# Performance work log

Measured on AMD Instinct MI355X. Metric: run time of the kernel, lower is better.

The kernel has to match this reference:

```python
import jax, jax.numpy as jnp
import numpy as np

# PaTH attention (training path, attention_mask=None):
#   score(t,s) = q_t^T (H_t H_{t-1} ... H_{s+1}) k_s,  H_i = I - beta_i w_i w_i^T (w_i unit-norm)
# computed in closed form via a UT/WY-style triangular solve, then causal softmax with
# FoX-style forget gate: logits += cumsum(logsigmoid(g))_t - cumsum(logsigmoid(g))_s.

NUM_HEADS = 32
HEAD_DIM = 64
CONV_K = 3
NEG_INF = -1e30


def _forward(hidden_states, Wq, Wk, Wv, Ww1, Ww2, conv_w, Wbt, bbt, Wg, bg, Wo):
    B, T, D = hidden_states.shape
    H, hd, Kc = NUM_HEADS, HEAD_DIM, CONV_K
    h = hidden_states
    q = h @ Wq                                   # [B,T,D]
    k = h @ Wk
    v = h @ Wv
    w = (h @ Ww1) @ Ww2                          # low-rank w_proj (rank 32)
    beta = jax.nn.sigmoid(h @ Wbt + bbt) * 2.0   # [B,T,H], in (0,2)
    g = jax.nn.log_sigmoid(h @ Wg + bg)          # [B,T,H] forget gate (log-space)
    # causal depthwise short conv (kernel 3, no bias) + silu on w
    wp = jnp.pad(w, ((0, 0), (Kc - 1, 0), (0, 0)))
    w = sum(wp[:, j:j + T, :] * conv_w[:, j] for j in range(Kc))
    w = jax.nn.silu(w)
    split = lambda x: x.reshape(B, T, H, hd)
    q, k, v, w = split(q), split(k), split(v), split(w)
    w = w * jax.lax.rsqrt(jnp.sum(w * w, axis=-1, keepdims=True))  # l2_norm per head
    # pairwise inner products, [B,H,T,S]
    Dqk = jnp.einsum('bthd,bshd->bhts', q, k)
    E = jnp.einsum('bthd,bshd->bhts', q, w)
    S = jnp.einsum('bthd,bshd->bhts', w, k)
    L = jnp.einsum('bthd,bshd->bhts', w, w)
    bcol = jnp.transpose(beta, (0, 2, 1))[:, :, None, :]  # beta_i indexed by column i
    strict = jnp.tril(jnp.ones((T, T), bool), -1)
    # C[t,s] = w_t^T (H_{t-1}...H_{s+1}) k_s solves (I + strict(L) diag(beta)) C = strict(S)
    M = jnp.eye(T, dtype=q.dtype) + jnp.where(strict, L * bcol, 0.0)
    rhs = jnp.where(strict, S, 0.0)
    C = jax.scipy.linalg.solve_triangular(M, rhs, lower=True, unit_diagonal=True)
    causal = jnp.tril(jnp.ones((T, T), bool))
    # A[t,s] = q_t^T k_s - sum_{s<i<=t} (q_t^T w_i) beta_i C[i,s]
    EB = jnp.where(causal, E, 0.0) * bcol
    A = Dqk - EB @ C
    G = jnp.cumsum(jnp.transpose(g, (0, 2, 1)), axis=-1)  # [B,H,T]
    logits = A * (hd ** -0.5) + G[..., :, None] - G[..., None, :]
    logits = jnp.where(causal, logits, NEG_INF)
    P = jax.nn.softmax(logits, axis=-1)
    o = jnp.einsum('bhts,bshd->bthd', P, v).reshape(B, T, D)
    return o @ Wo


def setup_inputs() -> dict:
    key = jax.random.key(0)
    ks = jax.random.split(key, 12)
    B, T, D, H, Kc = 1, 1024, 2048, NUM_HEADS, CONV_K
    r = lambda k, shape, scale: jax.random.normal(k, shape, dtype=jnp.float32) * scale
    s = D ** -0.5
    return {
        'hidden_states': r(ks[0], (B, T, D), 1.0),
        'Wq': r(ks[1], (D, D), s),
        'Wk': r(ks[2], (D, D), s),
        'Wv': r(ks[3], (D, D), s),
        'Ww1': r(ks[4], (D, 32), s),
        'Ww2': r(ks[5], (32, D), 32 ** -0.5),
        'conv_w': r(ks[6], (D, Kc), Kc ** -0.5),
        'Wbt': r(ks[7], (D, H), s),
        'bbt': r(ks[8], (H,), 1.0),
        'Wg': r(ks[9], (D, H), s),
        'bg': r(ks[10], (H,), 1.0),
        'Wo': r(ks[11], (D, D), s),
    }


def reference(hidden_states, Wq, Wk, Wv, Ww1, Ww2, conv_w, Wbt, bbt, Wg, bg, Wo):
    return _forward(hidden_states, Wq, Wk, Wv, Ww1, Ww2, conv_w, Wbt, bbt, Wg, bg, Wo)
```

## Files before the change

### kernel.cpp

```cpp
#include <hip/hip_runtime.h>
#include <hip/hip_bf16.h>

typedef __hip_bfloat16 bf16;
typedef unsigned short ushort_t;

#define T_  1024
#define D_  2048
#define H_  32
#define HD_ 64

static const size_t TT_ = (size_t)T_ * T_;
static const size_t TD_ = (size_t)T_ * D_;

__device__ __forceinline__ ushort_t f2bf(float v) {
    bf16 b = __float2bfloat16(v);
    return *(ushort_t*)&b;
}
__device__ __forceinline__ float bf2f(ushort_t u) {
    bf16 b = *(bf16*)&u;
    return __bfloat162float(b);
}

typedef __attribute__((ext_vector_type(8))) short frag8;
typedef __attribute__((ext_vector_type(4))) float f32x4;
typedef __attribute__((ext_vector_type(4))) unsigned short u16x4;
typedef __attribute__((ext_vector_type(8))) unsigned short u16x8;

#define MFMA16(a, b, c) __builtin_amdgcn_mfma_f32_16x16x32_bf16((a), (b), (c), 0, 0, 0)

template <int OUT>
__global__ __launch_bounds__(256) void mfma_gemm(
    const ushort_t* __restrict__ A, const ushort_t* __restrict__ Bt,
    void* __restrict__ Cout, void* __restrict__ Cout2, int M, int N, int K)
{
    __shared__ short Al[128 * 32];
    __shared__ short Bl[128 * 32];
    int tid = threadIdx.x;
    int w = tid >> 6, l = tid & 63;
    int row0 = blockIdx.y * 128, col0 = blockIdx.x * 128;
    int mq = (w >> 1) * 64, nq = (w & 1) * 64;
    int lm = l & 15, kq = l >> 4;
    f32x4 acc[4][4] = {};
    const ushort_t* Ap = A + (size_t)row0 * K;
    const ushort_t* Bp = Bt + (size_t)col0 * K;
    for (int kk = 0; kk < K; kk += 32) {
        __syncthreads();
#pragma unroll
        for (int r = 0; r < 2; r++) {
            int c = r * 256 + w * 64 + l;
            int row = c >> 2, kc = (c & 3) * 8;
            const ushort_t* ga = Ap + (size_t)row * K + kk + kc;
            const ushort_t* gb = Bp + (size_t)row * K + kk + kc;
            short* la = Al + (size_t)(r * 256 + w * 64) * 8;
            short* lb = Bl + (size_t)(r * 256 + w * 64) * 8;
            __builtin_amdgcn_global_load_lds((const __attribute__((address_space(1))) void*)ga,
                                             (__attribute__((address_space(3))) void*)la, 16, 0, 0);
            __builtin_amdgcn_global_load_lds((const __attribute__((address_space(1))) void*)gb,
                                             (__attribute__((address_space(3))) void*)lb, 16, 0, 0);
        }
        __builtin_amdgcn_s_waitcnt(0);
        __syncthreads();
        frag8 af[4], bfg[4];
#pragma unroll
        for (int i = 0; i < 4; i++)
            af[i] = *(const frag8*)&Al[(size_t)(mq + i * 16 + lm) * 32 + kq * 8];
#pragma unroll
        for (int j = 0; j < 4; j++)
            bfg[j] = *(const frag8*)&Bl[(size_t)(nq + j * 16 + lm) * 32 + kq * 8];
#pragma unroll
        for (int i = 0; i < 4; i++)
#pragma unroll
            for (int j = 0; j < 4; j++)
                acc[i][j] = MFMA16(af[i], bfg[j], acc[i][j]);
    }
#pragma unroll
    for (int i = 0; i < 4; i++)
#pragma unroll
        for (int j = 0; j < 4; j++)
#pragma unroll
            for (int r = 0; r < 4; r++) {
                int row = row0 + mq + i * 16 + kq * 4 + r;
                int col = col0 + nq + j * 16 + lm;
                float v = acc[i][j][r];
                if (OUT == 0) {
                    ((float*)Cout)[(size_t)row * N + col] = v;
                } else {
                    ushort_t* q = (ushort_t*)Cout;
                    int which = col >> 11, cl = col & 2047;
                    int hd = cl >> 6, d = cl & 63;
                    if (which == 0)
                        q[((size_t)hd * M + row) * 64 + d] = f2bf(v);
                    else if (which == 1)
                        q[(size_t)M * 2048 + ((size_t)hd * M + row) * 64 + d] = f2bf(v);
                    else if (which == 2)
                        q[(size_t)M * 4096 + ((size_t)hd * 64 + d) * M + row] = f2bf(v);
                    else
                        ((float*)Cout2)[(size_t)row * 128 + (col - 6144)] = v;
                }
            }
}

__global__ void transpose_convert(const float* __restrict__ W, ushort_t* __restrict__ Wt,
                                  int R, int Cc)
{
    __shared__ float tile[32][33];
    int bx = blockIdx.x * 32, by = blockIdx.y * 32;
    int tx = threadIdx.x, ty = threadIdx.y;
    for (int i = ty; i < 32; i += 8)
        tile[i][tx] = W[(size_t)(by + i) * Cc + bx + tx];
    __syncthreads();
    for (int i = ty; i < 32; i += 8)
        Wt[(size_t)(bx + i) * R + by + tx] = f2bf(tile[tx][i]);
}

__global__ void pack96(const float* __restrict__ Ww1, const float* __restrict__ Wbt,
                       const float* __restrict__ Wg, ushort_t* __restrict__ dst)
{
    int r = blockIdx.x;
    int k = blockIdx.y * 256 + threadIdx.x;
    float v = 0.f;
    if (r < 32)       v = Ww1[(size_t)k * 32 + r];
    else if (r < 64)  v = Wbt[(size_t)k * 32 + (r - 32)];
    else if (r < 96)  v = Wg[(size_t)k * 32 + (r - 64)];
    dst[(size_t)r * 2048 + k] = f2bf(v);
}

__global__ void convert_bf16(const float* __restrict__ in, ushort_t* __restrict__ out, int n)
{
    int i = blockIdx.x * 256 + threadIdx.x;
    if (i < n) out[i] = f2bf(in[i]);
}

__global__ void bg96(const float* __restrict__ s96, const float* __restrict__ bbt,
                     const float* __restrict__ bgp, ushort_t* __restrict__ w1bf,
                     float* __restrict__ betaB, float* __restrict__ Gb)
{
    int idx = blockIdx.x * 256 + threadIdx.x;
    int t = idx >> 7, o = idx & 127;
    if (o >= 96) return;
    float v = s96[(size_t)t * 128 + o];
    if (o < 32) {
        w1bf[(size_t)t * 32 + o] = f2bf(v);
    } else if (o < 64) {
        float xb = v + bbt[o - 32];
        betaB[(size_t)t * H_ + (o - 32)] = 2.f / (1.f + expf(-xb));
    } else {
        float xg = v + bgp[o - 64];
        Gb[(size_t)t * H_ + (o - 64)] =
            (xg >= 0.f) ? -log1pf(expf(-xg)) : (xg - log1pf(expf(xg)));
    }
}

__global__ void scan_g(float* __restrict__ G)
{
    int h = blockIdx.x;
    int tid = threadIdx.x;
    __shared__ float psum[256];
    float v[4];
    float s = 0.f;
#pragma unroll
    for (int r = 0; r < 4; r++) {
        v[r] = G[(size_t)(tid * 4 + r) * H_ + h];
        s += v[r];
    }
    psum[tid] = s;
    __syncthreads();
    for (int off = 1; off < 256; off <<= 1) {
        float t = (tid >= off) ? psum[tid - off] : 0.f;
        __syncthreads();
        psum[tid] += t;
        __syncthreads();
    }
    float run = (tid > 0) ? psum[tid - 1] : 0.f;
#pragma unroll
    for (int r = 0; r < 4; r++) {
        run += v[r];
        G[(size_t)(tid * 4 + r) * H_ + h] = run;
    }
}

__global__ void conv_silu_norm(const float* __restrict__ wr, const float* __restrict__ convw,
                               ushort_t* __restrict__ wh)
{
    int b = blockIdx.x;
    int t = b >> 5, h = b & 31;
    int d = threadIdx.x;
    int c = h * 64 + d;
    float c0 = convw[c * 3 + 0];
    float c1 = convw[c * 3 + 1];
    float c2 = convw[c * 3 + 2];
    float x = c2 * wr[(size_t)t * D_ + c];
    if (t >= 1) x += c1 * wr[(size_t)(t - 1) * D_ + c];
    if (t >= 2) x += c0 * wr[(size_t)(t - 2) * D_ + c];
    float y = x / (1.f + expf(-x));
    float ss = y * y;
    for (int off = 32; off > 0; off >>= 1) ss += __shfl_xor(ss, off, 64);
    wh[((size_t)h * T_ + t) * 64 + d] = f2bf(y * rsqrtf(ss));
}

__global__ __launch_bounds__(256) void pairdotLC(
    const ushort_t* __restrict__ kh, const ushort_t* __restrict__ wh,
    const float* __restrict__ betaB,
    ushort_t* __restrict__ ELb, ushort_t* __restrict__ Ct, int hs)
{
    int s0 = blockIdx.x * 64, t0 = blockIdx.y * 64, z = blockIdx.z;
    if (s0 > t0) return;
    int head = hs + z;
    const ushort_t* kb = kh + (size_t)head * T_ * 64;
    const ushort_t* wb = wh + (size_t)head * T_ * 64;
    ushort_t* Lz = ELb + (size_t)z * TT_;
    ushort_t* Cz = Ct + (size_t)z * TT_;
    int tid = threadIdx.x;
    int w = tid >> 6, l = tid & 63;
    int lm = l & 15, kq = l >> 4;
    int rowA = t0 + w * 16 + lm;
    f32x4 accL[4] = {}, accS[4] = {};
#pragma unroll
    for (int kk = 0; kk < 64; kk += 32) {
        frag8 aw = *(const frag8*)&wb[(size_t)rowA * 64 + kk + kq * 8];
#pragma unroll
        for (int j = 0; j < 4; j++) {
            int colr = s0 + j * 16 + lm;
            frag8 bw = *(const frag8*)&wb[(size_t)colr * 64 + kk + kq * 8];
            frag8 bk = *(const frag8*)&kb[(size_t)colr * 64 + kk + kq * 8];
            accL[j] = MFMA16(aw, bw, accL[j]);
            accS[j] = MFMA16(aw, bk, accS[j]);
        }
    }
    int m0 = w * 16 + kq * 4;
#pragma unroll
    for (int j = 0; j < 4; j++) {
        int s = s0 + j * 16 + lm;
        float beta = betaB[(size_t)s * H_ + head];
        ushort_t cl[4];
#pragma unroll
        for (int r = 0; r < 4; r++) {
            int t = t0 + m0 + r;
            Lz[(size_t)t * T_ + s] = f2bf((s < t) ? accL[j][r] * beta : 0.f);
            cl[r] = f2bf((s < t) ? accS[j][r] : 0.f);
        }
        *(u16x4*)&Cz[(size_t)s * T_ + t0 + m0] = *(u16x4*)cl;
    }
}

__global__ __launch_bounds__(256) void pairdotE(
    const ushort_t* __restrict__ qh, const ushort_t* __restrict__ wh,
    const float* __restrict__ betaB, ushort_t* __restrict__ ELb, int hs)
{
    int s0 = blockIdx.x * 64, t0 = blockIdx.y * 64, z = blockIdx.z;
    if (s0 > t0) return;
    int head = hs + z;
    const ushort_t* qb = qh + (size_t)head * T_ * 64;
    const ushort_t* wb = wh + (size_t)head * T_ * 64;
    ushort_t* Ez = ELb + (size_t)z * TT_;
    int tid = threadIdx.x;
    int w = tid >> 6, l = tid & 63;
    int lm = l & 15, kq = l >> 4;
    int rowA = t0 + w * 16 + lm;
    f32x4 accE[4] = {};
#pragma unroll
    for (int kk = 0; kk < 64; kk += 32) {
        frag8 aq = *(const frag8*)&qb[(size_t)rowA * 64 + kk + kq * 8];
#pragma unroll
        for (int j = 0; j < 4; j++) {
            frag8 bw = *(const frag8*)&wb[(size_t)(s0 + j * 16 + lm) * 64 + kk + kq * 8];
            accE[j] = MFMA16(aq, bw, accE[j]);
        }
    }
    int m0 = w * 16 + kq * 4;
#pragma unroll
    for (int j = 0; j < 4; j++) {
        int s = s0 + j * 16 + lm;
        float beta = betaB[(size_t)s * H_ + head];
#pragma unroll
        for (int r = 0; r < 4; r++) {
            int t = t0 + m0 + r;
            Ez[(size_t)t * T_ + s] = f2bf((s <= t) ? -accE[j][r] * beta : 0.f);
        }
    }
}

__global__ void diag_inv(const ushort_t* __restrict__ Lb, ushort_t* __restrict__ Minv)
{
    int bi = blockIdx.x, z = blockIdx.y;
    const ushort_t* Lh = Lb + (size_t)z * TT_;
    __shared__ float Nb[64][65];
    __shared__ float Xc[64][65];
    int tid = threadIdx.x;
    for (int i = tid; i < 4096; i += 64) {
        int r = i >> 6, c = i & 63;
        Nb[r][c] = (c < r) ? bf2f(Lh[(size_t)(bi * 64 + r) * T_ + bi * 64 + c]) : 0.f;
    }
    __syncthreads();
    int j = tid;
    for (int t = 0; t < 64; t++) {
        float v = (t == j) ? 1.f : 0.f;
        for (int i = j; i < t; i++) v -= Nb[t][i] * Xc[i][j];
        Xc[t][j] = v;
    }
    __syncthreads();
    ushort_t* Mo = Minv + ((size_t)z * 16 + bi) * 4096;
    for (int i = tid; i < 4096; i += 64) Mo[i] = f2bf(Xc[i >> 6][i & 63]);
}

__global__ __launch_bounds__(256) void solve_mfma(
    ushort_t* __restrict__ Ct, const ushort_t* __restrict__ Lb,
    const ushort_t* __restrict__ Minv)
{
    int ct = blockIdx.x, z = blockIdx.y;
    ushort_t* Cz = Ct + (size_t)z * TT_;
    const ushort_t* Lz = Lb + (size_t)z * TT_;
    __shared__ ushort_t Cl[64][136];
    __shared__ ushort_t Ll[64][136];
    __shared__ ushort_t Xbt[64][72];
    int tid = threadIdx.x;
    int w = tid >> 6, l = tid & 63;
    int lm = l & 15, kq = l >> 4;
    int s0 = ct * 64;
    int m0 = w * 16 + kq * 4;
    for (int bi = ct; bi < 16; bi++) {
        f32x4 acc[4] = {};
        for (int kkc = s0; kkc < bi * 64; kkc += 128) {
            int len = bi * 64 - kkc; if (len > 128) len = 128;
            int lsh = (len == 128) ? 4 : 3;
            __syncthreads();
            for (int i = tid; i < (64 << lsh); i += 256) {
                int r = i >> lsh, c = (i & ((1 << lsh) - 1)) * 8;
                *(u16x8*)&Cl[r][c] = *(const u16x8*)&Cz[(size_t)(s0 + r) * T_ + kkc + c];
                *(u16x8*)&Ll[r][c] = *(const u16x8*)&Lz[(size_t)(bi * 64 + r) * T_ + kkc + c];
            }
            __syncthreads();
            for (int kk2 = 0; kk2 < len; kk2 += 32) {
                frag8 a = *(const frag8*)&Ll[w * 16 + lm][kk2 + kq * 8];
#pragma unroll
                for (int j = 0; j < 4; j++) {
                    frag8 b = *(const frag8*)&Cl[j * 16 + lm][kk2 + kq * 8];
                    acc[j] = MFMA16(a, b, acc[j]);
                }
            }
        }
        __syncthreads();
#pragma unroll
        for (int j = 0; j < 4; j++) {
            int sc = s0 + j * 16 + lm;
            u16x4 rhs = *(const u16x4*)&Cz[(size_t)sc * T_ + bi * 64 + m0];
            ushort_t xb[4];
#pragma unroll
            for (int r = 0; r < 4; r++) xb[r] = f2bf(bf2f(rhs[r]) - acc[j][r]);
            *(u16x4*)&Xbt[j * 16 + lm][m0] = *(u16x4*)xb;
        }
        __syncthreads();
        f32x4 res[4] = {};
        const ushort_t* Mo = Minv + ((size_t)z * 16 + bi) * 4096;
#pragma unroll
        for (int kk = 0; kk < 64; kk += 32) {
            frag8 a = *(const frag8*)&Mo[(size_t)(w * 16 + lm) * 64 + kk + kq * 8];
#pragma unroll
            for (int j = 0; j < 4; j++) {
                frag8 b = *(const frag8*)&Xbt[j * 16 + lm][kk + kq * 8];
                res[j] = MFMA16(a, b, res[j]);
            }
        }
#pragma unroll
        for (int j = 0; j < 4; j++) {
            int sc = s0 + j * 16 + lm;
            ushort_t cr[4];
#pragma unroll
            for (int r = 0; r < 4; r++) cr[r] = f2bf(res[j][r]);
            *(u16x4*)&Cz[(size_t)sc * T_ + bi * 64 + m0] = *(u16x4*)cr;
        }
        __syncthreads();
    }
}

__global__ __launch_bounds__(256) void flash_attn(
    const ushort_t* __restrict__ qh, const ushort_t* __restrict__ kh,
    const ushort_t* __restrict__ vt, const ushort_t* __restrict__ Em,
    const ushort_t* __restrict__ Ct, const float* __restrict__ Gb,
    ushort_t* __restrict__ of, int hs)
{
    int tb = (int)gridDim.x - 1 - (int)blockIdx.x;
    int z = blockIdx.y;
    int t0 = tb * 64;
    int head = hs + z;
    const ushort_t* qb = qh + (size_t)head * T_ * 64;
    const ushort_t* kb = kh + (size_t)head * T_ * 64;
    const ushort_t* vb = vt + (size_t)head * 64 * T_;
    const ushort_t* Ez = Em + (size_t)z * TT_;
    const ushort_t* Cz = Ct + (size_t)z * TT_;
    __shared__ ushort_t Kl[64][72];
    __shared__ ushort_t Vl[64][72];
    __shared__ ushort_t Cl[64][72];
    __shared__ ushort_t El[64][72];
    __shared__ ushort_t Pl[4][16][72];
    int tid = threadIdx.x;
    int w = tid >> 6, l = tid & 63;
    int lm = l & 15, kq = l >> 4;
    int rowA = t0 + w * 16 + lm;
    int m0 = w * 16 + kq * 4;
    frag8 aq0 = *(const frag8*)&qb[(size_t)rowA * 64 + kq * 8];
    frag8 aq1 = *(const frag8*)&qb[(size_t)rowA * 64 + 32 + kq * 8];
    f32x4 o[4] = {};
    float mrow[4], lrow[4];
#pragma unroll
    for (int r = 0; r < 4; r++) { mrow[r] = -1e30f; lrow[r] = 0.f; }
    for (int st = 0; st <= tb; st++) {
        int s0 = st * 64;
        __syncthreads();
        for (int i = tid; i < 512; i += 256) {
            int r = i >> 3, c = (i & 7) * 8;
            *(u16x8*)&Kl[r][c] = *(const u16x8*)&kb[(size_t)(s0 + r) * 64 + c];
            *(u16x8*)&Vl[r][c] = *(const u16x8*)&vb[(size_t)r * T_ + s0 + c];
        }
        __syncthreads();
        f32x4 x[4] = {};
#pragma unroll
        for (int j = 0; j < 4; j++) {
            frag8 b0 = *(const frag8*)&Kl[j * 16 + lm][kq * 8];
            frag8 b1 = *(const frag8*)&Kl[j * 16 + lm][32 + kq * 8];
            x[j] = MFMA16(aq0, b0, x[j]);
            x[j] = MFMA16(aq1, b1, x[j]);
        }
        for (int kkc = s0; kkc < t0 + 64; kkc += 64) {
            __syncthreads();
            for (int i = tid; i < 512; i += 256) {
                int r = i >> 3, c = (i & 7) * 8;
                *(u16x8*)&Cl[r][c] = *(const u16x8*)&Cz[(size_t)(s0 + r) * T_ + kkc + c];
                *(u16x8*)&El[r][c] = *(const u16x8*)&Ez[(size_t)(t0 + r) * T_ + kkc + c];
            }
            __syncthreads();
#pragma unroll
            for (int kk2 = 0; kk2 < 64; kk2 += 32) {
                frag8 a = *(const frag8*)&El[w * 16 + lm][kk2 + kq * 8];
#pragma unroll
                for (int j = 0; j < 4; j++) {
                    frag8 b = *(const frag8*)&Cl[j * 16 + lm][kk2 + kq * 8];
                    x[j] = MFMA16(a, b, x[j]);
                }
            }
        }
        float lg[4][4];
#pragma unroll
        for (int j = 0; j < 4; j++) {
            int s = s0 + j * 16 + lm;
            float g = Gb[(size_t)s * H_ + head];
#pragma unroll
            for (int r = 0; r < 4; r++) {
                int t = t0 + m0 + r;
                lg[j][r] = (s <= t) ? (x[j][r] * 0.125f - g) : -1e30f;
            }
        }
        float rmax[4];
#pragma unroll
        for (int r = 0; r < 4; r++)
            rmax[r] = fmaxf(fmaxf(lg[0][r], lg[1][r]), fmaxf(lg[2][r], lg[3][r]));
#pragma unroll
        for (int d = 1; d < 16; d <<= 1)
#pragma unroll
            for (int r = 0; r < 4; r++) rmax[r] = fmaxf(rmax[r], __shfl_xor(rmax[r], d, 64));
        float mnew[4], alpha[4];
#pragma unroll
        for (int r = 0; r < 4; r++) {
            mnew[r] = fmaxf(mrow[r], rmax[r]);
            alpha[r] = __expf(mrow[r] - mnew[r]);
            mrow[r] = mnew[r];
        }
        float rsum[4] = {0.f, 0.f, 0.f, 0.f};
#pragma unroll
        for (int j = 0; j < 4; j++)
#pragma unroll
            for (int r = 0; r < 4; r++) {
                float p = __expf(lg[j][r] - mnew[r]);
                lg[j][r] = p;
                rsum[r] += p;
            }
#pragma unroll
        for (int d = 1; d < 16; d <<= 1)
#pragma unroll
            for (int r = 0; r < 4; r++) rsum[r] += __shfl_xor(rsum[r], d, 64);
#pragma unroll
        for (int r = 0; r < 4; r++) lrow[r] = lrow[r] * alpha[r] + rsum[r];
#pragma unroll
        for (int j = 0; j < 4; j++)
#pragma unroll
            for (int r = 0; r < 4; r++) o[j][r] *= alpha[r];
#pragma unroll
        for (int j = 0; j < 4; j++)
#pragma unroll
            for (int r = 0; r < 4; r++)
                Pl[w][kq * 4 + r][j * 16 + lm] = f2bf(lg[j][r]);
#pragma unroll
        for (int j = 0; j < 4; j++) {
            frag8 b0 = *(const frag8*)&Vl[j * 16 + lm][kq * 8];
            frag8 b1 = *(const frag8*)&Vl[j * 16 + lm][32 + kq * 8];
            frag8 a0 = *(const frag8*)&Pl[w][lm][kq * 8];
            frag8 a1 = *(const frag8*)&Pl[w][lm][32 + kq * 8];
            o[j] = MFMA16(a0, b0, o[j]);
            o[j] = MFMA16(a1, b1, o[j]);
        }
    }
#pragma unroll
    for (int j = 0; j < 4; j++) {
        int col = head * 64 + j * 16 + lm;
#pragma unroll
        for (int r = 0; r < 4; r++) {
            int t = t0 + m0 + r;
            of[(size_t)t * D_ + col] = f2bf(o[j][r] / lrow[r]);
        }
    }
}

extern "C" void kernel_launch(void* const* d_in, const int* in_sizes, int n_in,
                              void* d_out, int out_size, void* d_ws, size_t ws_size,
                              hipStream_t stream)
{
    const float* h     = (const float*)d_in[0];
    const float* Wq    = (const float*)d_in[1];
    const float* Wk    = (const float*)d_in[2];
    const float* Wv    = (const float*)d_in[3];
    const float* Ww1   = (const float*)d_in[4];
    const float* Ww2   = (const float*)d_in[5];
    const float* convw = (const float*)d_in[6];
    const float* Wbt   = (const float*)d_in[7];
    const float* bbt   = (const float*)d_in[8];
    const float* Wg    = (const float*)d_in[9];
    const float* bgp   = (const float*)d_in[10];
    const float* Wo    = (const float*)d_in[11];
    float* out = (float*)d_out;

    float* ws = (float*)d_ws;
    size_t off = 0;
    auto allocF = [&](size_t nf) { float* p = ws + off; off += (nf + 1023) & ~(size_t)1023; return p; };

    float*    wr    = allocF(TD_);
    float*    s96   = allocF((size_t)T_ * 128);
    float*    betaB = allocF((size_t)T_ * H_);
    float*    Gb    = allocF((size_t)T_ * H_);
    ushort_t* h_bf  = (ushort_t*)allocF(TD_ / 2);
    ushort_t* of_bf = h_bf;
    ushort_t* w1bf  = (ushort_t*)allocF((size_t)T_ * 32 / 2);
    ushort_t* Ww2t  = (ushort_t*)allocF((size_t)D_ * 32 / 2);
    ushort_t* Wtc   = (ushort_t*)allocF((size_t)6272 * D_ / 2);
    ushort_t* qkv   = (ushort_t*)allocF((size_t)3 * TD_ / 2);
    ushort_t* qh    = qkv;
    ushort_t* kh    = qkv + TD_;
    ushort_t* vt    = qkv + 2 * TD_;
    ushort_t* wh    = (ushort_t*)allocF(TD_ / 2);

    size_t fixedF = off;
    size_t capF = ws_size / 4;
    size_t perHead = TT_ + ((size_t)16 * 4096) / 2 + 2048;
    int NH = 32;
    while (NH > 1 && fixedF + (size_t)NH * perHead > capF) NH >>= 1;
    ushort_t* ELb = (ushort_t*)allocF((size_t)NH * TT_ / 2);
    ushort_t* Ct  = (ushort_t*)allocF((size_t)NH * TT_ / 2);
    ushort_t* Mv  = (ushort_t*)allocF((size_t)NH * 16 * 4096 / 2);

    dim3 blk(256);
    dim3 tcvB(32, 8);
    dim3 tcvG(D_ / 32, D_ / 32);

    convert_bf16<<<dim3((TD_ + 255) / 256), blk, 0, stream>>>(h, h_bf, (int)TD_);
    transpose_convert<<<tcvG, tcvB, 0, stream>>>(Wq, Wtc, D_, D_);
    transpose_convert<<<tcvG, tcvB, 0, stream>>>(Wk, Wtc + (size_t)D_ * D_, D_, D_);
    transpose_convert<<<tcvG, tcvB, 0, stream>>>(Wv, Wtc + (size_t)2 * D_ * D_, D_, D_);
    pack96<<<dim3(128, 8), blk, 0, stream>>>(Ww1, Wbt, Wg, Wtc + (size_t)3 * D_ * D_);
    mfma_gemm<3><<<dim3(6272 / 128, T_ / 128), blk, 0, stream>>>(
        h_bf, Wtc, qkv, s96, T_, 6272, D_);

    bg96<<<dim3(T_ * 128 / 256), blk, 0, stream>>>(s96, bbt, bgp, w1bf, betaB, Gb);
    scan_g<<<dim3(H_), blk, 0, stream>>>(Gb);
    transpose_convert<<<dim3(D_ / 32, 1), tcvB, 0, stream>>>(Ww2, Ww2t, 32, D_);
    mfma_gemm<0><<<dim3(D_ / 128, T_ / 128), blk, 0, stream>>>(
        w1bf, Ww2t, wr, nullptr, T_, D_, 32);
    conv_silu_norm<<<dim3(T_ * H_), dim3(64), 0, stream>>>(wr, convw, wh);

    int nChunks = H_ / NH;
    for (int c = 0; c < nChunks; c++) {
        int hs = c * NH;
        pairdotLC<<<dim3(16, 16, NH), blk, 0, stream>>>(kh, wh, betaB, ELb, Ct, hs);
        diag_inv<<<dim3(16, NH), dim3(64), 0, stream>>>(ELb, Mv);
        solve_mfma<<<dim3(16, NH), blk, 0, stream>>>(Ct, ELb, Mv);
        pairdotE<<<dim3(16, 16, NH), blk, 0, stream>>>(qh, wh, betaB, ELb, hs);
        flash_attn<<<dim3(16, NH), blk, 0, stream>>>(qh, kh, vt, ELb, Ct, Gb, of_bf, hs);
    }

    transpose_convert<<<tcvG, tcvB, 0, stream>>>(Wo, Wtc, D_, D_);
    mfma_gemm<0><<<dim3(D_ / 128, T_ / 128), blk, 0, stream>>>(
        of_bf, Wtc, out, nullptr, T_, D_, D_);
}
```

Baseline: 903.1 us.

## Split flash attention over key tiles, fuse E computation, add combine pass

Replaces the per-query-tile sequential flash attention with a split-K scheme. Each block handles one (query tile, key tile) pair, computes E = -beta*q·w on the fly instead of reading a materialized E matrix, and writes its partial output plus row max and sum. A new combine kernel merges the partials. This removes the pairdotE pass and the heavy load imbalance of the old 16×NH grid, at the cost of recomputing q·w per key tile and extra partial-output traffic.

```diff
diff --git a/kernel.cpp b/kernel.cpp
--- a/kernel.cpp
+++ b/kernel.cpp
@@ -243,43 +243,6 @@
     }
 }
 
-__global__ __launch_bounds__(256) void pairdotE(
-    const ushort_t* __restrict__ qh, const ushort_t* __restrict__ wh,
-    const float* __restrict__ betaB, ushort_t* __restrict__ ELb, int hs)
-{
-    int s0 = blockIdx.x * 64, t0 = blockIdx.y * 64, z = blockIdx.z;
-    if (s0 > t0) return;
-    int head = hs + z;
-    const ushort_t* qb = qh + (size_t)head * T_ * 64;
-    const ushort_t* wb = wh + (size_t)head * T_ * 64;
-    ushort_t* Ez = ELb + (size_t)z * TT_;
-    int tid = threadIdx.x;
-    int w = tid >> 6, l = tid & 63;
-    int lm = l & 15, kq = l >> 4;
-    int rowA = t0 + w * 16 + lm;
-    f32x4 accE[4] = {};
-#pragma unroll
-    for (int kk = 0; kk < 64; kk += 32) {
-        frag8 aq = *(const frag8*)&qb[(size_t)rowA * 64 + kk + kq * 8];
-#pragma unroll
-        for (int j = 0; j < 4; j++) {
-            frag8 bw = *(const frag8*)&wb[(size_t)(s0 + j * 16 + lm) * 64 + kk + kq * 8];
-            accE[j] = MFMA16(aq, bw, accE[j]);
-        }
-    }
-    int m0 = w * 16 + kq * 4;
-#pragma unroll
-    for (int j = 0; j < 4; j++) {
-        int s = s0 + j * 16 + lm;
-        float beta = betaB[(size_t)s * H_ + head];
-#pragma unroll
-        for (int r = 0; r < 4; r++) {
-            int t = t0 + m0 + r;
-            Ez[(size_t)t * T_ + s] = f2bf((s <= t) ? -accE[j][r] * beta : 0.f);
-        }
-    }
-}
-
 __global__ void diag_inv(const ushort_t* __restrict__ Lb, ushort_t* __restrict__ Minv)
 {
     int bi = blockIdx.x, z = blockIdx.y;
@@ -373,141 +336,176 @@
     }
 }
 
-__global__ __launch_bounds__(256) void flash_attn(
+__global__ __launch_bounds__(256) void flash_split(
     const ushort_t* __restrict__ qh, const ushort_t* __restrict__ kh,
-    const ushort_t* __restrict__ vt, const ushort_t* __restrict__ Em,
-    const ushort_t* __restrict__ Ct, const float* __restrict__ Gb,
-    ushort_t* __restrict__ of, int hs)
-{
-    int tb = (int)gridDim.x - 1 - (int)blockIdx.x;
-    int z = blockIdx.y;
-    int t0 = tb * 64;
+    const ushort_t* __restrict__ vt, const ushort_t* __restrict__ wh,
+    const ushort_t* __restrict__ Ct, const float* __restrict__ betaB,
+    const float* __restrict__ Gb, ushort_t* __restrict__ Op,
+    float* __restrict__ ml, int hs)
+{
+    int st = blockIdx.x, tb = blockIdx.y, z = blockIdx.z;
+    if (st > tb) return;
+    int t0 = tb * 64, s0 = st * 64;
     int head = hs + z;
     const ushort_t* qb = qh + (size_t)head * T_ * 64;
     const ushort_t* kb = kh + (size_t)head * T_ * 64;
     const ushort_t* vb = vt + (size_t)head * 64 * T_;
-    const ushort_t* Ez = Em + (size_t)z * TT_;
+    const ushort_t* wb = wh + (size_t)head * T_ * 64;
     const ushort_t* Cz = Ct + (size_t)z * TT_;
     __shared__ ushort_t Kl[64][72];
     __shared__ ushort_t Vl[64][72];
+    __shared__ ushort_t Wl[64][72];
     __shared__ ushort_t Cl[64][72];
-    __shared__ ushort_t El[64][72];
     __shared__ ushort_t Pl[4][16][72];
     int tid = threadIdx.x;
     int w = tid >> 6, l = tid & 63;
     int lm = l & 15, kq = l >> 4;
     int rowA = t0 + w * 16 + lm;
     int m0 = w * 16 + kq * 4;
+    for (int i = tid; i < 512; i += 256) {
+        int r = i >> 3, c = (i & 7) * 8;
+        *(u16x8*)&Kl[r][c] = *(const u16x8*)&kb[(size_t)(s0 + r) * 64 + c];
+        *(u16x8*)&Vl[r][c] = *(const u16x8*)&vb[(size_t)r * T_ + s0 + c];
+    }
     frag8 aq0 = *(const frag8*)&qb[(size_t)rowA * 64 + kq * 8];
     frag8 aq1 = *(const frag8*)&qb[(size_t)rowA * 64 + 32 + kq * 8];
-    f32x4 o[4] = {};
-    float mrow[4], lrow[4];
-#pragma unroll
-    for (int r = 0; r < 4; r++) { mrow[r] = -1e30f; lrow[r] = 0.f; }
-    for (int st = 0; st <= tb; st++) {
-        int s0 = st * 64;
+    __syncthreads();
+    f32x4 x[4] = {};
+#pragma unroll
+    for (int j = 0; j < 4; j++) {
+        frag8 b0 = *(const frag8*)&Kl[j * 16 + lm][kq * 8];
+        frag8 b1 = *(const frag8*)&Kl[j * 16 + lm][32 + kq * 8];
+        x[j] = MFMA16(aq0, b0, x[j]);
+        x[j] = MFMA16(aq1, b1, x[j]);
+    }
+    for (int kc = s0; kc < t0 + 64; kc += 64) {
         __syncthreads();
         for (int i = tid; i < 512; i += 256) {
             int r = i >> 3, c = (i & 7) * 8;
-            *(u16x8*)&Kl[r][c] = *(const u16x8*)&kb[(size_t)(s0 + r) * 64 + c];
-            *(u16x8*)&Vl[r][c] = *(const u16x8*)&vb[(size_t)r * T_ + s0 + c];
-        }
-        __syncthreads();
-        f32x4 x[4] = {};
-#pragma unroll
-        for (int j = 0; j < 4; j++) {
-            frag8 b0 = *(const frag8*)&Kl[j * 16 + lm][kq * 8];
-            frag8 b1 = *(const frag8*)&Kl[j * 16 + lm][32 + kq * 8];
-            x[j] = MFMA16(aq0, b0, x[j]);
-            x[j] = MFMA16(aq1, b1, x[j]);
-        }
-        for (int kkc = s0; kkc < t0 + 64; kkc += 64) {
-            __syncthreads();
-            for (int i = tid; i < 512; i += 256) {
-                int r = i >> 3, c = (i & 7) * 8;
-                *(u16x8*)&Cl[r][c] = *(const u16x8*)&Cz[(size_t)(s0 + r) * T_ + kkc + c];
-                *(u16x8*)&El[r][c] = *(const u16x8*)&Ez[(size_t)(t0 + r) * T_ + kkc + c];
-            }
-            __syncthreads();
-#pragma unroll
-            for (int kk2 = 0; kk2 < 64; kk2 += 32) {
-                frag8 a = *(const frag8*)&El[w * 16 + lm][kk2 + kq * 8];
-#pragma unroll
-                for (int j = 0; j < 4; j++) {
-                    frag8 b = *(const frag8*)&Cl[j * 16 + lm][kk2 + kq * 8];
-                    x[j] = MFMA16(a, b, x[j]);
-                }
-            }
-        }
-        float lg[4][4];
-#pragma unroll
-        for (int j = 0; j < 4; j++) {
-            int s = s0 + j * 16 + lm;
-            float g = Gb[(size_t)s * H_ + head];
+            *(u16x8*)&Wl[r][c] = *(const u16x8*)&wb[(size_t)(kc + r) * 64 + c];
+            *(u16x8*)&Cl[r][c] = *(const u16x8*)&Cz[(size_t)(s0 + r) * T_ + kc + c];
+        }
+        __syncthreads();
+        f32x4 eq[4] = {};
+#pragma unroll
+        for (int jj = 0; jj < 4; jj++) {
+            frag8 b0 = *(const frag8*)&Wl[jj * 16 + lm][kq * 8];
+            frag8 b1 = *(const frag8*)&Wl[jj * 16 + lm][32 + kq * 8];
+            eq[jj] = MFMA16(aq0, b0, eq[jj]);
+            eq[jj] = MFMA16(aq1, b1, eq[jj]);
+        }
+#pragma unroll
+        for (int jj = 0; jj < 4; jj++) {
+            int k = kc + jj * 16 + lm;
+            float beta = betaB[(size_t)k * H_ + head];
 #pragma unroll
             for (int r = 0; r < 4; r++) {
                 int t = t0 + m0 + r;
-                lg[j][r] = (s <= t) ? (x[j][r] * 0.125f - g) : -1e30f;
+                float v = (k <= t) ? -eq[jj][r] * beta : 0.f;
+                Pl[w][kq * 4 + r][jj * 16 + lm] = f2bf(v);
             }
         }
-        float rmax[4];
-#pragma unroll
-        for (int r = 0; r < 4; r++)
-            rmax[r] = fmaxf(fmaxf(lg[0][r], lg[1][r]), fmaxf(lg[2][r], lg[3][r]));
-#pragma unroll
-        for (int d = 1; d < 16; d <<= 1)
-#pragma unroll
-            for (int r = 0; r < 4; r++) rmax[r] = fmaxf(rmax[r], __shfl_xor(rmax[r], d, 64));
-        float mnew[4], alpha[4];
-#pragma unroll
-        for (int r = 0; r < 4; r++) {
-            mnew[r] = fmaxf(mrow[r], rmax[r]);
-            alpha[r] = __expf(mrow[r] - mnew[r]);
-            mrow[r] = mnew[r];
-        }
-        float rsum[4] = {0.f, 0.f, 0.f, 0.f};
-#pragma unroll
-        for (int j = 0; j < 4; j++)
-#pragma unroll
-            for (int r = 0; r < 4; r++) {
-                float p = __expf(lg[j][r] - mnew[r]);
-                lg[j][r] = p;
-                rsum[r] += p;
+#pragma unroll
+        for (int kk2 = 0; kk2 < 64; kk2 += 32) {
+            frag8 a = *(const frag8*)&Pl[w][lm][kk2 + kq * 8];
+#pragma unroll
+            for (int j = 0; j < 4; j++) {
+                frag8 b = *(const frag8*)&Cl[j * 16 + lm][kk2 + kq * 8];
+                x[j] = MFMA16(a, b, x[j]);
             }
-#pragma unroll
-        for (int d = 1; d < 16; d <<= 1)
-#pragma unroll
-            for (int r = 0; r < 4; r++) rsum[r] += __shfl_xor(rsum[r], d, 64);
-#pragma unroll
-        for (int r = 0; r < 4; r++) lrow[r] = lrow[r] * alpha[r] + rsum[r];
-#pragma unroll
-        for (int j = 0; j < 4; j++)
-#pragma unroll
-            for (int r = 0; r < 4; r++) o[j][r] *= alpha[r];
-#pragma unroll
-        for (int j = 0; j < 4; j++)
-#pragma unroll
-            for (int r = 0; r < 4; r++)
-                Pl[w][kq * 4 + r][j * 16 + lm] = f2bf(lg[j][r]);
-#pragma unroll
-        for (int j = 0; j < 4; j++) {
-            frag8 b0 = *(const frag8*)&Vl[j * 16 + lm][kq * 8];
-            frag8 b1 = *(const frag8*)&Vl[j * 16 + lm][32 + kq * 8];
-            frag8 a0 = *(const frag8*)&Pl[w][lm][kq * 8];
-            frag8 a1 = *(const frag8*)&Pl[w][lm][32 + kq * 8];
-            o[j] = MFMA16(a0, b0, o[j]);
-            o[j] = MFMA16(a1, b1, o[j]);
-        }
-    }
+        }
+    }
+    float lg[4][4];
 #pragma unroll
     for (int j = 0; j < 4; j++) {
-        int col = head * 64 + j * 16 + lm;
+        int s = s0 + j * 16 + lm;
+        float g = Gb[(size_t)s * H_ + head];
 #pragma unroll
         for (int r = 0; r < 4; r++) {
             int t = t0 + m0 + r;
-            of[(size_t)t * D_ + col] = f2bf(o[j][r] / lrow[r]);
-        }
-    }
+            lg[j][r] = (s <= t) ? (x[j][r] * 0.125f - g) : -1e30f;
+        }
+    }
+    float mrow[4];
+#pragma unroll
+    for (int r = 0; r < 4; r++)
+        mrow[r] = fmaxf(fmaxf(lg[0][r], lg[1][r]), fmaxf(lg[2][r], lg[3][r]));
+#pragma unroll
+    for (int d = 1; d < 16; d <<= 1)
+#pragma unroll
+        for (int r = 0; r < 4; r++) mrow[r] = fmaxf(mrow[r], __shfl_xor(mrow[r], d, 64));
+    float lrow[4] = {0.f, 0.f, 0.f, 0.f};
+#pragma unroll
+    for (int j = 0; j < 4; j++)
+#pragma unroll
+        for (int r = 0; r < 4; r++) {
+            float p = __expf(lg[j][r] - mrow[r]);
+            lg[j][r] = p;
+            lrow[r] += p;
+        }
+#pragma unroll
+    for (int d = 1; d < 16; d <<= 1)
+#pragma unroll
+        for (int r = 0; r < 4; r++) lrow[r] += __shfl_xor(lrow[r], d, 64);
+#pragma unroll
+    for (int j = 0; j < 4; j++)
+#pragma unroll
+        for (int r = 0; r < 4; r++)
+            Pl[w][kq * 4 + r][j * 16 + lm] = f2bf(lg[j][r]);
+    f32x4 o[4] = {};
+#pragma unroll
+    for (int j = 0; j < 4; j++) {
+        frag8 b0 = *(const frag8*)&Vl[j * 16 + lm][kq * 8];
+        frag8 b1 = *(const frag8*)&Vl[j * 16 + lm][32 + kq * 8];
+        frag8 a0 = *(const frag8*)&Pl[w][lm][kq * 8];
+        frag8 a1 = *(const frag8*)&Pl[w][lm][32 + kq * 8];
+        o[j] = MFMA16(a0, b0, o[j]);
+        o[j] = MFMA16(a1, b1, o[j]);
+    }
+    size_t pbase = (((size_t)z * 16 + tb) * 16 + st) * 4096;
+#pragma unroll
+    for (int j = 0; j < 4; j++)
+#pragma unroll
+        for (int r = 0; r < 4; r++)
+            Op[pbase + (size_t)(m0 + r) * 64 + j * 16 + lm] = f2bf(o[j][r]);
+    if (lm == 0) {
+        size_t mbase = (((size_t)z * 16 + tb) * 16 + st) * 128;
+#pragma unroll
+        for (int r = 0; r < 4; r++) {
+            ml[mbase + m0 + r] = mrow[r];
+            ml[mbase + 64 + m0 + r] = lrow[r];
+        }
+    }
+}
+
+__global__ __launch_bounds__(256) void combine(
+    const ushort_t* __restrict__ Op, const float* __restrict__ ml,
+    ushort_t* __restrict__ of, int hs)
+{
+    int tb = blockIdx.x, z = blockIdx.y;
+    int head = hs + z;
+    int tid = threadIdx.x;
+    int row = tid >> 2, cg = (tid & 3) * 16;
+    size_t mb0 = (((size_t)z * 16 + tb) * 16) * 128;
+    float M = -1e30f;
+    for (int st = 0; st <= tb; st++)
+        M = fmaxf(M, ml[mb0 + (size_t)st * 128 + row]);
+    float acc[16] = {};
+    float lsum = 0.f;
+    for (int st = 0; st <= tb; st++) {
+        float mp = ml[mb0 + (size_t)st * 128 + row];
+        float lp = ml[mb0 + (size_t)st * 128 + 64 + row];
+        float sc = __expf(mp - M);
+        lsum += lp * sc;
+        const ushort_t* op = Op + (((size_t)z * 16 + tb) * 16 + st) * 4096 + (size_t)row * 64 + cg;
+#pragma unroll
+        for (int i = 0; i < 16; i++) acc[i] += bf2f(op[i]) * sc;
+    }
+    float inv = 1.f / lsum;
+    int t = tb * 64 + row;
+    ushort_t* dst = of + (size_t)t * D_ + (size_t)head * 64 + cg;
+#pragma unroll
+    for (int i = 0; i < 16; i++) dst[i] = f2bf(acc[i] * inv);
 }
 
 extern "C" void kernel_launch(void* const* d_in, const int* in_sizes, int n_in,
@@ -549,12 +547,13 @@
 
     size_t fixedF = off;
     size_t capF = ws_size / 4;
-    size_t perHead = TT_ + ((size_t)16 * 4096) / 2 + 2048;
+    size_t perHead = TT_ + ((size_t)16 * 4096) / 2 + (size_t)16 * 16 * 128 + 2048;
     int NH = 32;
     while (NH > 1 && fixedF + (size_t)NH * perHead > capF) NH >>= 1;
     ushort_t* ELb = (ushort_t*)allocF((size_t)NH * TT_ / 2);
     ushort_t* Ct  = (ushort_t*)allocF((size_t)NH * TT_ / 2);
     ushort_t* Mv  = (ushort_t*)allocF((size_t)NH * 16 * 4096 / 2);
+    float*    mlB = allocF((size_t)NH * 16 * 16 * 128);
 
     dim3 blk(256);
     dim3 tcvB(32, 8);
@@ -581,8 +580,9 @@
         pairdotLC<<<dim3(16, 16, NH), blk, 0, stream>>>(kh, wh, betaB, ELb, Ct, hs);
         diag_inv<<<dim3(16, NH), dim3(64), 0, stream>>>(ELb, Mv);
         solve_mfma<<<dim3(16, NH), blk, 0, stream>>>(Ct, ELb, Mv);
-        pairdotE<<<dim3(16, 16, NH), blk, 0, stream>>>(qh, wh, betaB, ELb, hs);
-        flash_attn<<<dim3(16, NH), blk, 0, stream>>>(qh, kh, vt, ELb, Ct, Gb, of_bf, hs);
+        flash_split<<<dim3(16, 16, NH), blk, 0, stream>>>(
+            qh, kh, vt, wh, Ct, betaB, Gb, ELb, mlB, hs);
+        combine<<<dim3(16, NH), blk, 0, stream>>>(ELb, mlB, of_bf, hs);
     }
 
     transpose_convert<<<tcvG, tcvB, 0, stream>>>(Wo, Wtc, D_, D_);
```

After: 900.3 us. Within noise of the previous version (-0.3%).
